# Optimization experiments

Hardware: AMD Instinct MI355X
Metric: run time of the kernel (lower is better)

## Reference

```python
import jax, jax.numpy as jnp
import numpy as np

TOP_K = 2
AUX_COEF = 0.001


def setup_inputs() -> dict:
    key = jax.random.key(0)
    ks = jax.random.split(key, 5)
    B, S, H, I, E = 4, 2048, 1024, 4096, 8
    return {
        "hidden_states": jax.random.normal(ks[0], (B, S, H), dtype=jnp.float32),
        "router_w": jax.random.normal(ks[1], (H, E), dtype=jnp.float32) * 0.02,
        "w_gate": jax.random.normal(ks[2], (E, H, I), dtype=jnp.float32) * 0.02,
        "w_up": jax.random.normal(ks[3], (E, H, I), dtype=jnp.float32) * 0.02,
        "w_down": jax.random.normal(ks[4], (E, I, H), dtype=jnp.float32) * 0.02,
    }


def reference(hidden_states, router_w, w_gate, w_up, w_down):
    B, S, H = hidden_states.shape
    E = router_w.shape[1]
    x = jnp.clip(hidden_states, -10.0, 10.0)          # [B,S,H]
    xf = x.reshape(-1, H)                              # [T,H]
    T = xf.shape[0]

    # --- token-choice router (fp32) ---
    logits = xf.astype(jnp.float32) @ router_w         # [T,E]
    z_loss = jnp.mean(jax.nn.logsumexp(logits, axis=-1) ** 2)
    probs = jax.nn.softmax(logits, axis=-1)            # [T,E]
    top_w, top_i = jax.lax.top_k(probs, TOP_K)         # [T,K]
    top_w = top_w / jnp.sum(top_w, axis=-1, keepdims=True)
    # load-balance loss: aux * E * sum_e f_e * P_e
    assign = jax.nn.one_hot(top_i, E, dtype=jnp.float32).sum(axis=1)  # [T,E]
    frac_tokens = assign.mean(axis=0) / TOP_K
    mean_probs = probs.mean(axis=0)
    lb_loss = AUX_COEF * E * jnp.sum(frac_tokens * mean_probs)

    # --- dense per-expert SwiGLU MLP, then gather selected outputs ---
    expert_outs = []
    for e in range(E):  # small fixed loop over experts
        gate = xf @ w_gate[e]                          # [T,I]
        up = xf @ w_up[e]                              # [T,I]
        expert_outs.append((jax.nn.silu(gate) * up) @ w_down[e])  # [T,H]
    outs = jnp.stack(expert_outs, axis=0)              # [E,T,H]

    gathered = outs[top_i, jnp.arange(T)[:, None], :]  # [T,K,H]
    out = jnp.einsum("tk,tkh->th", top_w.astype(x.dtype), gathered)
    out = jnp.clip(out, -10.0, 10.0).reshape(B, S, H)
    return out, lb_loss, z_loss
```

## Files before the change

### kernel.cpp

```cpp
#include <hip/hip_runtime.h>
#include <stdint.h>

#define TOKENS 8192
#define HDIM 1024
#define IDIM 4096
#define NEXP 8
#define MPAD 17408
#define MTILES 136

typedef float f32x4 __attribute__((ext_vector_type(4)));
typedef __bf16 bf16x8 __attribute__((ext_vector_type(8)));

static __device__ __forceinline__ uint16_t f2bf(float f) {
  uint32_t u = __builtin_bit_cast(uint32_t, f);
  return (uint16_t)((u + 0x7fffu + ((u >> 16) & 1u)) >> 16);
}
static __device__ __forceinline__ uint32_t pack2(float a, float b) {
  return (uint32_t)f2bf(a) | ((uint32_t)f2bf(b) << 16);
}
static __device__ __forceinline__ float bf2f(uint32_t h) {
  return __builtin_bit_cast(float, h << 16);
}
#define SWZ(r) (((r) ^ ((r) >> 3)) & 7u)
static __device__ __forceinline__ void load_lds16(const void* g, void* l) {
  __builtin_amdgcn_global_load_lds(
      (const __attribute__((address_space(1))) uint32_t*)(uintptr_t)g,
      (__attribute__((address_space(3))) uint32_t*)(uintptr_t)l, 16, 0, 0);
}

__global__ __launch_bounds__(256) void router_kernel(
    const float* __restrict__ x, const float* __restrict__ rw,
    uint16_t* __restrict__ xb, float2* __restrict__ topw, int2* __restrict__ tope,
    int* __restrict__ cnt_slots, float* __restrict__ psum_slots, float* __restrict__ zsum_slots) {
  const int tid = threadIdx.x;
  const int lane = tid & 63, wid = tid >> 6;
  const int t = blockIdx.x * 4 + wid;

  const float* xrow = x + (size_t)t * HDIM + lane * 16;
  float xc[16];
#pragma unroll
  for (int i = 0; i < 4; ++i) {
    float4 v = *(const float4*)(xrow + i * 4);
    xc[i * 4 + 0] = fminf(fmaxf(v.x, -10.f), 10.f);
    xc[i * 4 + 1] = fminf(fmaxf(v.y, -10.f), 10.f);
    xc[i * 4 + 2] = fminf(fmaxf(v.z, -10.f), 10.f);
    xc[i * 4 + 3] = fminf(fmaxf(v.w, -10.f), 10.f);
  }
  uint4 o0, o1;
  o0.x = pack2(xc[0], xc[1]);   o0.y = pack2(xc[2], xc[3]);
  o0.z = pack2(xc[4], xc[5]);   o0.w = pack2(xc[6], xc[7]);
  o1.x = pack2(xc[8], xc[9]);   o1.y = pack2(xc[10], xc[11]);
  o1.z = pack2(xc[12], xc[13]); o1.w = pack2(xc[14], xc[15]);
  uint4* dst = (uint4*)(xb + (size_t)t * HDIM + lane * 16);
  dst[0] = o0; dst[1] = o1;

  float acc[8];
#pragma unroll
  for (int e = 0; e < 8; ++e) acc[e] = 0.f;
  const float* rwp = rw + (size_t)(lane * 16) * NEXP;
#pragma unroll
  for (int i = 0; i < 16; ++i) {
    float xi = xc[i];
    float4 a = *(const float4*)(rwp + i * 8);
    float4 b = *(const float4*)(rwp + i * 8 + 4);
    acc[0] += xi * a.x; acc[1] += xi * a.y; acc[2] += xi * a.z; acc[3] += xi * a.w;
    acc[4] += xi * b.x; acc[5] += xi * b.y; acc[6] += xi * b.z; acc[7] += xi * b.w;
  }
#pragma unroll
  for (int s = 1; s < 64; s <<= 1) {
#pragma unroll
    for (int e = 0; e < 8; ++e) acc[e] += __shfl_xor(acc[e], s);
  }

  __shared__ float sp[8]; __shared__ int sc[8]; __shared__ float sz;
  if (tid < 8) { sp[tid] = 0.f; sc[tid] = 0; }
  if (tid == 0) sz = 0.f;
  __syncthreads();

  if (lane == 0) {
    float mx = acc[0];
#pragma unroll
    for (int e = 1; e < 8; ++e) mx = fmaxf(mx, acc[e]);
    float p[8]; float s = 0.f;
#pragma unroll
    for (int e = 0; e < 8; ++e) { p[e] = expf(acc[e] - mx); s += p[e]; }
    float inv = 1.f / s;
#pragma unroll
    for (int e = 0; e < 8; ++e) p[e] *= inv;
    float lse = mx + logf(s);
    int e0 = 0; float b0 = p[0];
#pragma unroll
    for (int e = 1; e < 8; ++e) if (p[e] > b0) { b0 = p[e]; e0 = e; }
    int e1 = (e0 == 0) ? 1 : 0; float b1 = (e0 == 0) ? p[1] : p[0];
#pragma unroll
    for (int e = 0; e < 8; ++e) if (e != e0 && p[e] > b1) { b1 = p[e]; e1 = e; }
    float wn = 1.f / (b0 + b1);
    topw[t] = make_float2(b0 * wn, b1 * wn);
    tope[t] = make_int2(e0, e1);
#pragma unroll
    for (int e = 0; e < 8; ++e) atomicAdd(&sp[e], p[e]);
    atomicAdd(&sc[e0], 1); atomicAdd(&sc[e1], 1);
    atomicAdd(&sz, lse * lse);
  }
  __syncthreads();
  int slot = blockIdx.x & 63;
  if (tid < 8) {
    atomicAdd(&cnt_slots[slot * 8 + tid], sc[tid]);
    atomicAdd(&psum_slots[slot * 8 + tid], sp[tid]);
  }
  if (tid == 0) atomicAdd(&zsum_slots[slot], sz);
}

__global__ void scan_kernel(const int* __restrict__ cnt_slots,
                            const float* __restrict__ psum_slots,
                            const float* __restrict__ zsum_slots,
                            int* __restrict__ seg, int* __restrict__ fill_cnt,
                            float* __restrict__ out_sc) {
  const int tid = threadIdx.x;
  __shared__ int c[8]; __shared__ float ps[8];
  if (tid < 8) {
    int s = 0; float f = 0.f;
    for (int k = 0; k < 64; ++k) { s += cnt_slots[k * 8 + tid]; f += psum_slots[k * 8 + tid]; }
    c[tid] = s; ps[tid] = f; fill_cnt[tid] = 0;
  }
  __syncthreads();
  if (tid == 0) {
    int off = 0;
    for (int e = 0; e < 8; ++e) { seg[e] = off; off += (c[e] + 127) & ~127; }
    seg[8] = off;
    float lb = 0.f;
    for (int e = 0; e < 8; ++e)
      lb += ((float)c[e] / (2.0f * (float)TOKENS)) * (ps[e] / (float)TOKENS);
    lb *= 0.001f * (float)NEXP;
    float z = 0.f;
    for (int k = 0; k < 64; ++k) z += zsum_slots[k];
    out_sc[0] = lb;
    out_sc[1] = z / (float)TOKENS;
  }
}

__global__ __launch_bounds__(256) void fill_kernel(
    const int2* __restrict__ tope, const int* __restrict__ seg,
    int* __restrict__ fill_cnt, int* __restrict__ rowtok) {
  const int t = blockIdx.x * 256 + threadIdx.x;
  const int lane = threadIdx.x & 63;
  const int2 te = tope[t];
#pragma unroll
  for (int k = 0; k < 2; ++k) {
    const int e = k ? te.y : te.x;
    int pos = 0;
    for (int ee = 0; ee < 8; ++ee) {
      unsigned long long mask = __ballot(e == ee);
      if (e == ee) {
        unsigned long long below = mask & ((lane == 0) ? 0ull : (~0ull >> (64 - lane)));
        int nbelow = __popcll(below);
        int leader = __ffsll((unsigned long long)mask) - 1;
        int base = 0;
        if (lane == leader) base = atomicAdd(&fill_cnt[ee], __popcll(mask));
        base = __shfl(base, leader);
        pos = seg[ee] + base + nbelow;
      }
    }
    rowtok[pos] = t * 2 + k;
  }
}

__global__ __launch_bounds__(256) void convert_kernel(
    const float* __restrict__ w_gate, const float* __restrict__ w_up,
    const float* __restrict__ w_down, uint16_t* __restrict__ wgT,
    uint16_t* __restrict__ wuT, uint16_t* __restrict__ wdT) {
  __shared__ uint64_t tt[64][17];
  const int tid = threadIdx.x;
  const int z = blockIdx.y;
  const int bx = blockIdx.x;
  const float* src; uint16_t* dst; int R, C, tr, tc;
  if (z < 16) {
    R = 1024; C = 4096; tr = bx >> 6; tc = bx & 63;
    int e = z & 7;
    src = (z < 8 ? w_gate : w_up) + (size_t)e * 1024 * 4096;
    dst = (z < 8 ? wgT : wuT) + (size_t)e * 1024 * 4096;
  } else {
    R = 4096; C = 1024; tr = bx >> 4; tc = bx & 15;
    int e = z - 16;
    src = w_down + (size_t)e * 4096 * 1024;
    dst = wdT + (size_t)e * 4096 * 1024;
  }
  const int i = tid >> 4, j = tid & 15;
  float4 v0 = *(const float4*)(src + (size_t)(tr * 64 + 4 * i + 0) * C + tc * 64 + 4 * j);
  float4 v1 = *(const float4*)(src + (size_t)(tr * 64 + 4 * i + 1) * C + tc * 64 + 4 * j);
  float4 v2 = *(const float4*)(src + (size_t)(tr * 64 + 4 * i + 2) * C + tc * 64 + 4 * j);
  float4 v3 = *(const float4*)(src + (size_t)(tr * 64 + 4 * i + 3) * C + tc * 64 + 4 * j);
  tt[4 * j + 0][i] = (uint64_t)pack2(v0.x, v1.x) | ((uint64_t)pack2(v2.x, v3.x) << 32);
  tt[4 * j + 1][i] = (uint64_t)pack2(v0.y, v1.y) | ((uint64_t)pack2(v2.y, v3.y) << 32);
  tt[4 * j + 2][i] = (uint64_t)pack2(v0.z, v1.z) | ((uint64_t)pack2(v2.z, v3.z) << 32);
  tt[4 * j + 3][i] = (uint64_t)pack2(v0.w, v1.w) | ((uint64_t)pack2(v2.w, v3.w) << 32);
  __syncthreads();
#pragma unroll
  for (int it = 0; it < 2; ++it) {
    int idx = it * 256 + tid;
    int c = idx >> 3, h = idx & 7;
    uint64_t a = tt[c][2 * h], b = tt[c][2 * h + 1];
    uint4 v;
    v.x = (uint32_t)a; v.y = (uint32_t)(a >> 32);
    v.z = (uint32_t)b; v.w = (uint32_t)(b >> 32);
    *(uint4*)(dst + (size_t)(tc * 64 + c) * R + tr * 64 + h * 8) = v;
  }
}

static __device__ __forceinline__ int xcd_swz(int b, int nwg) {
  int q = nwg >> 3, r = nwg & 7;
  int xcd = b & 7;
  int base = (xcd < r) ? xcd * (q + 1) : r * (q + 1) + (xcd - r) * q;
  return base + (b >> 3);
}

__global__ __launch_bounds__(256, 2) void gemm1_kernel(
    const uint16_t* __restrict__ xb, const uint16_t* __restrict__ wgT,
    const uint16_t* __restrict__ wuT, const int* __restrict__ rowtok,
    const int* __restrict__ seg, uint16_t* __restrict__ hbuf, int mt0) {
  __shared__ __align__(16) char smem[49152];
  const int tid = threadIdx.x;
  const int lane = tid & 63, wid = tid >> 6;
  const int ct = (int)gridDim.y;
  const int b = (int)(blockIdx.y * gridDim.x + blockIdx.x);
  const int wg_lin = xcd_swz(b, 32 * ct);
  const int iblk = wg_lin / ct;
  const int mrel = wg_lin % ct;
  const int mtile = mt0 + mrel;
  const int row0 = mtile * 128;
  if (row0 >= seg[8]) return;
  int e = 0;
  while (row0 >= seg[e + 1]) ++e;
  const uint16_t* wgp = wgT + (size_t)e * HDIM * IDIM;
  const uint16_t* wup = wuT + (size_t)e * HDIM * IDIM;
  const int icol0 = iblk * 128;

  const uint32_t c8 = lane & 7;
  uintptr_t asrc[4], gsrc[4], usrc[4];
#pragma unroll
  for (int j = 0; j < 4; ++j) {
    uint32_t m = (uint32_t)(wid * 32 + j * 8 + (lane >> 3));
    int rt = rowtok[row0 + m];
    int tok = (rt < 0) ? 0 : (rt >> 1);
    uint32_t sw = (c8 ^ SWZ(m)) * 16;
    asrc[j] = (uintptr_t)(xb + (size_t)tok * HDIM) + sw;
    gsrc[j] = (uintptr_t)(wgp + (size_t)(icol0 + m) * HDIM) + sw;
    usrc[j] = (uintptr_t)(wup + (size_t)(icol0 + m) * HDIM) + sw;
  }

  f32x4 accg[4][4] = {}; f32x4 accu[4][4] = {};

  for (int kt = 0; kt < HDIM; kt += 64) {
    __syncthreads();
#pragma unroll
    for (int j = 0; j < 4; ++j) {
      load_lds16((const void*)(asrc[j] + (size_t)kt * 2), smem + wid * 4096 + j * 1024);
      load_lds16((const void*)(gsrc[j] + (size_t)kt * 2), smem + 16384 + wid * 4096 + j * 1024);
      load_lds16((const void*)(usrc[j] + (size_t)kt * 2), smem + 32768 + wid * 4096 + j * 1024);
    }
    __syncthreads();
    const uint32_t g = lane >> 4, l15 = lane & 15;
#pragma unroll
    for (int q = 0; q < 2; ++q) {
      bf16x8 af[4];
#pragma unroll
      for (int mi = 0; mi < 4; ++mi) {
        uint32_t m = (uint32_t)((wid >> 1) * 64 + mi * 16 + l15);
        af[mi] = *(const bf16x8*)(smem + m * 128 + (((uint32_t)(q * 4) + g) ^ SWZ(m)) * 16);
      }
      bf16x8 bg[4], bu[4];
#pragma unroll
      for (int ni = 0; ni < 4; ++ni) {
        uint32_t n = (uint32_t)((wid & 1) * 64 + ni * 16 + l15);
        uint32_t off = n * 128 + (((uint32_t)(q * 4) + g) ^ SWZ(n)) * 16;
        bg[ni] = *(const bf16x8*)(smem + 16384 + off);
        bu[ni] = *(const bf16x8*)(smem + 32768 + off);
      }
#pragma unroll
      for (int mi = 0; mi < 4; ++mi)
#pragma unroll
        for (int ni = 0; ni < 4; ++ni) {
          accg[mi][ni] = __builtin_amdgcn_mfma_f32_16x16x32_bf16(af[mi], bg[ni], accg[mi][ni], 0, 0, 0);
          accu[mi][ni] = __builtin_amdgcn_mfma_f32_16x16x32_bf16(af[mi], bu[ni], accu[mi][ni], 0, 0, 0);
        }
    }
  }
  __syncthreads();
  uint16_t* epi = (uint16_t*)smem;
  const int wr = wid >> 1, wc = wid & 1;
#pragma unroll
  for (int mi = 0; mi < 4; ++mi)
#pragma unroll
    for (int ni = 0; ni < 4; ++ni)
#pragma unroll
      for (int r = 0; r < 4; ++r) {
        float gv = accg[mi][ni][r], uv = accu[mi][ni][r];
        float hv = gv * uv * __frcp_rn(1.0f + __expf(-gv));
        int m = wr * 64 + mi * 16 + (lane >> 4) * 4 + r;
        int n = wc * 64 + ni * 16 + (lane & 15);
        epi[m * 136 + n] = f2bf(hv);
      }
  __syncthreads();
  const int hrow0 = (mtile - mt0) * 128;
  const int m = tid >> 1;
#pragma unroll
  for (int j = 0; j < 8; ++j) {
    int ch = (tid & 1) + j * 2;
    uint4 v = *(const uint4*)(smem + m * 272 + ch * 16);
    *(uint4*)(hbuf + ((size_t)(hrow0 + m)) * IDIM + icol0 + ch * 8) = v;
  }
}

__global__ __launch_bounds__(256, 2) void gemm2_kernel(
    const uint16_t* __restrict__ hbuf, const uint16_t* __restrict__ wdT,
    const int* __restrict__ rowtok, const int* __restrict__ seg,
    uint16_t* __restrict__ pairbuf, int mt0) {
  __shared__ __align__(16) char smem[34816];
  const int tid = threadIdx.x;
  const int lane = tid & 63, wid = tid >> 6;
  const int ct = (int)gridDim.y;
  const int b = (int)(blockIdx.y * gridDim.x + blockIdx.x);
  const int wg_lin = xcd_swz(b, 8 * ct);
  const int nblk = wg_lin / ct;
  const int mrel = wg_lin % ct;
  const int mtile = mt0 + mrel;
  const int row0 = mtile * 128;
  if (row0 >= seg[8]) return;
  int e = 0;
  while (row0 >= seg[e + 1]) ++e;
  const uint16_t* wdp = wdT + (size_t)e * IDIM * HDIM;
  const int ncol0 = nblk * 128;
  const int hrow0 = (mtile - mt0) * 128;

  const uint32_t c8 = lane & 7;
  uintptr_t asrc[4], bsrc[4];
#pragma unroll
  for (int j = 0; j < 4; ++j) {
    uint32_t m = (uint32_t)(wid * 32 + j * 8 + (lane >> 3));
    uint32_t sw = (c8 ^ SWZ(m)) * 16;
    asrc[j] = (uintptr_t)(hbuf + (size_t)(hrow0 + m) * IDIM) + sw;
    bsrc[j] = (uintptr_t)(wdp + (size_t)(ncol0 + m) * IDIM) + sw;
  }

  f32x4 acc[4][4] = {};

  for (int kt = 0; kt < IDIM; kt += 64) {
    __syncthreads();
#pragma unroll
    for (int j = 0; j < 4; ++j) {
      load_lds16((const void*)(asrc[j] + (size_t)kt * 2), smem + wid * 4096 + j * 1024);
      load_lds16((const void*)(bsrc[j] + (size_t)kt * 2), smem + 16384 + wid * 4096 + j * 1024);
    }
    __syncthreads();
    const uint32_t g = lane >> 4, l15 = lane & 15;
#pragma unroll
    for (int q = 0; q < 2; ++q) {
      bf16x8 af[4];
#pragma unroll
      for (int mi = 0; mi < 4; ++mi) {
        uint32_t m = (uint32_t)((wid >> 1) * 64 + mi * 16 + l15);
        af[mi] = *(const bf16x8*)(smem + m * 128 + (((uint32_t)(q * 4) + g) ^ SWZ(m)) * 16);
      }
      bf16x8 bf[4];
#pragma unroll
      for (int ni = 0; ni < 4; ++ni) {
        uint32_t n = (uint32_t)((wid & 1) * 64 + ni * 16 + l15);
        bf[ni] = *(const bf16x8*)(smem + 16384 + n * 128 + (((uint32_t)(q * 4) + g) ^ SWZ(n)) * 16);
      }
#pragma unroll
      for (int mi = 0; mi < 4; ++mi)
#pragma unroll
        for (int ni = 0; ni < 4; ++ni)
          acc[mi][ni] = __builtin_amdgcn_mfma_f32_16x16x32_bf16(af[mi], bf[ni], acc[mi][ni], 0, 0, 0);
    }
  }
  __syncthreads();
  uint16_t* epi = (uint16_t*)smem;
  const int wr = wid >> 1, wc = wid & 1;
#pragma unroll
  for (int mi = 0; mi < 4; ++mi)
#pragma unroll
    for (int ni = 0; ni < 4; ++ni)
#pragma unroll
      for (int r = 0; r < 4; ++r) {
        int m = wr * 64 + mi * 16 + (lane >> 4) * 4 + r;
        int n = wc * 64 + ni * 16 + (lane & 15);
        epi[m * 136 + n] = f2bf(acc[mi][ni][r]);
      }
  __syncthreads();
  const int m = tid >> 1;
  const int rt = rowtok[row0 + m];
  if (rt >= 0) {
#pragma unroll
    for (int j = 0; j < 8; ++j) {
      int ch = (tid & 1) + j * 2;
      uint4 v = *(const uint4*)(smem + m * 272 + ch * 16);
      *(uint4*)(pairbuf + (size_t)rt * HDIM + ncol0 + ch * 8) = v;
    }
  }
}

__global__ __launch_bounds__(256) void combine_kernel(
    const uint16_t* __restrict__ pairbuf, const float2* __restrict__ topw,
    float* __restrict__ out) {
  size_t i = (size_t)blockIdx.x * 256 + threadIdx.x;
  int t = (int)(i >> 7);
  int ch = (int)(i & 127);
  float2 w = topw[t];
  const uint16_t* p0 = pairbuf + (size_t)(t * 2) * HDIM + ch * 8;
  uint4 a = *(const uint4*)p0;
  uint4 b = *(const uint4*)(p0 + HDIM);
  float o[8];
  uint32_t au[4] = {a.x, a.y, a.z, a.w};
  uint32_t bu[4] = {b.x, b.y, b.z, b.w};
#pragma unroll
  for (int j = 0; j < 4; ++j) {
    float v0 = w.x * bf2f(au[j] & 0xffffu) + w.y * bf2f(bu[j] & 0xffffu);
    float v1 = w.x * bf2f(au[j] >> 16) + w.y * bf2f(bu[j] >> 16);
    o[j * 2 + 0] = fminf(fmaxf(v0, -10.f), 10.f);
    o[j * 2 + 1] = fminf(fmaxf(v1, -10.f), 10.f);
  }
  float* op = out + (size_t)t * HDIM + ch * 8;
  float4 w0 = {o[0], o[1], o[2], o[3]};
  float4 w1 = {o[4], o[5], o[6], o[7]};
  *(float4*)op = w0;
  *(float4*)(op + 4) = w1;
}

extern "C" void kernel_launch(void* const* d_in, const int* in_sizes, int n_in,
                              void* d_out, int out_size, void* d_ws, size_t ws_size,
                              hipStream_t stream) {
  (void)in_sizes; (void)n_in; (void)out_size;
  const float* x = (const float*)d_in[0];
  const float* rw = (const float*)d_in[1];
  const float* w_gate = (const float*)d_in[2];
  const float* w_up = (const float*)d_in[3];
  const float* w_down = (const float*)d_in[4];
  float* out = (float*)d_out;

  char* ws = (char*)d_ws;
  size_t off = 0;
  auto alloc = [&](size_t n) { char* p = ws + off; off += (n + 255) & ~(size_t)255; return p; };
  uint16_t* xb = (uint16_t*)alloc((size_t)TOKENS * HDIM * 2);
  float2* topw = (float2*)alloc((size_t)TOKENS * 8);
  int2* tope = (int2*)alloc((size_t)TOKENS * 8);
  int* rowtok = (int*)alloc((size_t)MPAD * 4);
  int* seg = (int*)alloc(16 * 4);
  int* fill_cnt = (int*)alloc(8 * 4);
  int* cnt_slots = (int*)alloc(64 * 8 * 4);
  float* psum_slots = (float*)alloc(64 * 8 * 4);
  float* zsum_slots = (float*)alloc(64 * 4);
  uint16_t* pairbuf = (uint16_t*)alloc((size_t)TOKENS * 2 * HDIM * 2);
  uint16_t* wgT = (uint16_t*)alloc((size_t)NEXP * HDIM * IDIM * 2);
  uint16_t* wuT = (uint16_t*)alloc((size_t)NEXP * HDIM * IDIM * 2);
  uint16_t* wdT = (uint16_t*)alloc((size_t)NEXP * IDIM * HDIM * 2);
  uint16_t* hbuf = (uint16_t*)(ws + off);
  size_t avail = (ws_size > off) ? (ws_size - off) : 0;
  long tiles_fit = (long)(avail / (128ull * IDIM * 2));
  int chunk = (tiles_fit >= MTILES) ? MTILES : (tiles_fit < 1 ? 1 : (int)tiles_fit);

  hipMemsetAsync(cnt_slots, 0, 64 * 8 * 4, stream);
  hipMemsetAsync(psum_slots, 0, 64 * 8 * 4, stream);
  hipMemsetAsync(zsum_slots, 0, 64 * 4, stream);
  hipMemsetAsync(rowtok, 0xFF, (size_t)MPAD * 4, stream);

  convert_kernel<<<dim3(1024, 24), 256, 0, stream>>>(w_gate, w_up, w_down, wgT, wuT, wdT);
  router_kernel<<<TOKENS / 4, 256, 0, stream>>>(x, rw, xb, topw, tope,
                                                cnt_slots, psum_slots, zsum_slots);
  scan_kernel<<<1, 64, 0, stream>>>(cnt_slots, psum_slots, zsum_slots, seg, fill_cnt,
                                    out + (size_t)TOKENS * HDIM);
  fill_kernel<<<TOKENS / 256, 256, 0, stream>>>(tope, seg, fill_cnt, rowtok);

  for (int mt0 = 0; mt0 < MTILES; mt0 += chunk) {
    int ct = (MTILES - mt0 < chunk) ? (MTILES - mt0) : chunk;
    gemm1_kernel<<<dim3(IDIM / 128, ct), 256, 0, stream>>>(xb, wgT, wuT, rowtok, seg, hbuf, mt0);
    gemm2_kernel<<<dim3(HDIM / 128, ct), 256, 0, stream>>>(hbuf, wdT, rowtok, seg, pairbuf, mt0);
  }
  combine_kernel<<<(TOKENS * HDIM / 8) / 256, 256, 0, stream>>>(pairbuf, topw, out);
}
```

Baseline: 740.3 us.

## Double-buffer LDS tiles with async global_load_lds prefetch in both expert GEMMs

Replaces the single-buffered K=64 load/sync/compute loops in the gate-up and down GEMMs with a two-stage ping-pong pipeline over K=32 tiles. The next tile is issued with global_load_lds right after fragments are read, using vmcnt waits and raw barriers, and s_setprio is raised around the MFMA block. The LDS swizzle changes to a 4-chunk pattern to fit the narrower 64-byte rows. The aim is to hide global memory latency behind MFMA work. The cost is more barriers per unit of K and tighter manual scheduling, which must be correct for the buffer-reuse hazards.

```diff
diff --git a/kernel.cpp b/kernel.cpp
--- a/kernel.cpp
+++ b/kernel.cpp
@@ -21,12 +21,19 @@
 static __device__ __forceinline__ float bf2f(uint32_t h) {
   return __builtin_bit_cast(float, h << 16);
 }
-#define SWZ(r) (((r) ^ ((r) >> 3)) & 7u)
+#define SWZ4(r) (((r) >> 1) & 3u)
 static __device__ __forceinline__ void load_lds16(const void* g, void* l) {
   __builtin_amdgcn_global_load_lds(
       (const __attribute__((address_space(1))) uint32_t*)(uintptr_t)g,
       (__attribute__((address_space(3))) uint32_t*)(uintptr_t)l, 16, 0, 0);
 }
+static __device__ __forceinline__ bf16x8 rdfrag(const char* base, uint32_t row, uint32_t g) {
+  return *(const bf16x8*)(base + row * 64 + ((g ^ SWZ4(row)) * 16));
+}
+#define WAITV(n) asm volatile("s_waitcnt vmcnt(" #n ")" ::: "memory")
+#define WAITL0 asm volatile("s_waitcnt lgkmcnt(0)" ::: "memory")
+#define BAR __builtin_amdgcn_s_barrier()
+#define SCHEDB __builtin_amdgcn_sched_barrier(0)
 
 __global__ __launch_bounds__(256) void router_kernel(
     const float* __restrict__ x, const float* __restrict__ rw,
@@ -235,56 +242,78 @@
   const uint16_t* wup = wuT + (size_t)e * HDIM * IDIM;
   const int icol0 = iblk * 128;
 
-  const uint32_t c8 = lane & 7;
-  uintptr_t asrc[4], gsrc[4], usrc[4];
-#pragma unroll
-  for (int j = 0; j < 4; ++j) {
-    uint32_t m = (uint32_t)(wid * 32 + j * 8 + (lane >> 3));
-    int rt = rowtok[row0 + m];
-    int tok = (rt < 0) ? 0 : (rt >> 1);
-    uint32_t sw = (c8 ^ SWZ(m)) * 16;
-    asrc[j] = (uintptr_t)(xb + (size_t)tok * HDIM) + sw;
-    gsrc[j] = (uintptr_t)(wgp + (size_t)(icol0 + m) * HDIM) + sw;
-    usrc[j] = (uintptr_t)(wup + (size_t)(icol0 + m) * HDIM) + sw;
-  }
+  const uint32_t r0 = (uint32_t)(wid * 32 + (lane >> 2));
+  const uint32_t r1 = r0 + 16;
+  const uint32_t cc0 = ((lane & 3u) ^ SWZ4(r0)) * 16;
+  const uint32_t cc1 = ((lane & 3u) ^ SWZ4(r1)) * 16;
+  int rt0 = rowtok[row0 + r0]; int tok0 = (rt0 < 0) ? 0 : (rt0 >> 1);
+  int rt1 = rowtok[row0 + r1]; int tok1 = (rt1 < 0) ? 0 : (rt1 >> 1);
+  const uintptr_t a0 = (uintptr_t)(xb + (size_t)tok0 * HDIM) + cc0;
+  const uintptr_t a1 = (uintptr_t)(xb + (size_t)tok1 * HDIM) + cc1;
+  const uintptr_t g0 = (uintptr_t)(wgp + (size_t)(icol0 + r0) * HDIM) + cc0;
+  const uintptr_t g1 = (uintptr_t)(wgp + (size_t)(icol0 + r1) * HDIM) + cc1;
+  const uintptr_t u0 = (uintptr_t)(wup + (size_t)(icol0 + r0) * HDIM) + cc0;
+  const uintptr_t u1 = (uintptr_t)(wup + (size_t)(icol0 + r1) * HDIM) + cc1;
+  const uint32_t ldsA = (uint32_t)(wid * 2048);
 
   f32x4 accg[4][4] = {}; f32x4 accu[4][4] = {};
 
-  for (int kt = 0; kt < HDIM; kt += 64) {
-    __syncthreads();
-#pragma unroll
-    for (int j = 0; j < 4; ++j) {
-      load_lds16((const void*)(asrc[j] + (size_t)kt * 2), smem + wid * 4096 + j * 1024);
-      load_lds16((const void*)(gsrc[j] + (size_t)kt * 2), smem + 16384 + wid * 4096 + j * 1024);
-      load_lds16((const void*)(usrc[j] + (size_t)kt * 2), smem + 32768 + wid * 4096 + j * 1024);
-    }
-    __syncthreads();
-    const uint32_t g = lane >> 4, l15 = lane & 15;
-#pragma unroll
-    for (int q = 0; q < 2; ++q) {
-      bf16x8 af[4];
-#pragma unroll
-      for (int mi = 0; mi < 4; ++mi) {
-        uint32_t m = (uint32_t)((wid >> 1) * 64 + mi * 16 + l15);
-        af[mi] = *(const bf16x8*)(smem + m * 128 + (((uint32_t)(q * 4) + g) ^ SWZ(m)) * 16);
-      }
-      bf16x8 bg[4], bu[4];
-#pragma unroll
-      for (int ni = 0; ni < 4; ++ni) {
-        uint32_t n = (uint32_t)((wid & 1) * 64 + ni * 16 + l15);
-        uint32_t off = n * 128 + (((uint32_t)(q * 4) + g) ^ SWZ(n)) * 16;
-        bg[ni] = *(const bf16x8*)(smem + 16384 + off);
-        bu[ni] = *(const bf16x8*)(smem + 32768 + off);
-      }
-#pragma unroll
-      for (int mi = 0; mi < 4; ++mi)
-#pragma unroll
-        for (int ni = 0; ni < 4; ++ni) {
-          accg[mi][ni] = __builtin_amdgcn_mfma_f32_16x16x32_bf16(af[mi], bg[ni], accg[mi][ni], 0, 0, 0);
-          accu[mi][ni] = __builtin_amdgcn_mfma_f32_16x16x32_bf16(af[mi], bu[ni], accu[mi][ni], 0, 0, 0);
-        }
-    }
-  }
+#define G1_ISSUE(t, buf)                                                        \
+  {                                                                             \
+    char* B_ = smem + (buf) * 24576;                                            \
+    size_t o_ = (size_t)(t) * 64;                                               \
+    load_lds16((const void*)(a0 + o_), B_ + ldsA);                              \
+    load_lds16((const void*)(a1 + o_), B_ + ldsA + 1024);                       \
+    load_lds16((const void*)(g0 + o_), B_ + 8192 + ldsA);                       \
+    load_lds16((const void*)(g1 + o_), B_ + 8192 + ldsA + 1024);                \
+    load_lds16((const void*)(u0 + o_), B_ + 16384 + ldsA);                      \
+    load_lds16((const void*)(u1 + o_), B_ + 16384 + ldsA + 1024);               \
+  }
+
+  const uint32_t g = lane >> 4, l15 = lane & 15;
+  const uint32_t mrow = (uint32_t)((wid >> 1) * 64) + l15;
+  const uint32_t nrow = (uint32_t)((wid & 1) * 64) + l15;
+
+#define G1_PHASE(buf)                                                           \
+  {                                                                             \
+    const char* B_ = smem + (buf) * 24576;                                      \
+    bf16x8 af[4], bg[4], bu[4];                                                 \
+    _Pragma("unroll") for (int mi = 0; mi < 4; ++mi)                            \
+        af[mi] = rdfrag(B_, mrow + mi * 16, g);                                 \
+    _Pragma("unroll") for (int ni = 0; ni < 4; ++ni) {                          \
+      bg[ni] = rdfrag(B_ + 8192, nrow + ni * 16, g);                            \
+      bu[ni] = rdfrag(B_ + 16384, nrow + ni * 16, g);                           \
+    }                                                                           \
+    WAITL0; SCHEDB;                                                             \
+    BAR; SCHEDB;                                                                \
+    ISSUE_NEXT;                                                                 \
+    SCHEDB;                                                                     \
+    __builtin_amdgcn_s_setprio(1);                                              \
+    _Pragma("unroll") for (int mi = 0; mi < 4; ++mi)                            \
+        _Pragma("unroll") for (int ni = 0; ni < 4; ++ni) {                      \
+      accg[mi][ni] = __builtin_amdgcn_mfma_f32_16x16x32_bf16(af[mi], bg[ni], accg[mi][ni], 0, 0, 0); \
+      accu[mi][ni] = __builtin_amdgcn_mfma_f32_16x16x32_bf16(af[mi], bu[ni], accu[mi][ni], 0, 0, 0); \
+    }                                                                           \
+    __builtin_amdgcn_s_setprio(0);                                              \
+  }
+
+  const int NT = HDIM / 32;
+  WAITV(0);
+  G1_ISSUE(0, 0);
+  G1_ISSUE(1, 1);
+  for (int t = 0; t < NT - 1; ++t) {
+    WAITV(6); BAR; SCHEDB;
+#define ISSUE_NEXT if (t + 2 < NT) G1_ISSUE(t + 2, t & 1)
+    G1_PHASE(t & 1);
+#undef ISSUE_NEXT
+  }
+  {
+    WAITV(0); BAR; SCHEDB;
+#define ISSUE_NEXT
+    G1_PHASE((NT - 1) & 1);
+#undef ISSUE_NEXT
+  }
+
   __syncthreads();
   uint16_t* epi = (uint16_t*)smem;
   const int wr = wid >> 1, wc = wid & 1;
@@ -332,48 +361,68 @@
   const int ncol0 = nblk * 128;
   const int hrow0 = (mtile - mt0) * 128;
 
-  const uint32_t c8 = lane & 7;
-  uintptr_t asrc[4], bsrc[4];
-#pragma unroll
-  for (int j = 0; j < 4; ++j) {
-    uint32_t m = (uint32_t)(wid * 32 + j * 8 + (lane >> 3));
-    uint32_t sw = (c8 ^ SWZ(m)) * 16;
-    asrc[j] = (uintptr_t)(hbuf + (size_t)(hrow0 + m) * IDIM) + sw;
-    bsrc[j] = (uintptr_t)(wdp + (size_t)(ncol0 + m) * IDIM) + sw;
-  }
+  const uint32_t r0 = (uint32_t)(wid * 32 + (lane >> 2));
+  const uint32_t r1 = r0 + 16;
+  const uint32_t cc0 = ((lane & 3u) ^ SWZ4(r0)) * 16;
+  const uint32_t cc1 = ((lane & 3u) ^ SWZ4(r1)) * 16;
+  const uintptr_t a0 = (uintptr_t)(hbuf + (size_t)(hrow0 + r0) * IDIM) + cc0;
+  const uintptr_t a1 = (uintptr_t)(hbuf + (size_t)(hrow0 + r1) * IDIM) + cc1;
+  const uintptr_t b0 = (uintptr_t)(wdp + (size_t)(ncol0 + r0) * IDIM) + cc0;
+  const uintptr_t b1 = (uintptr_t)(wdp + (size_t)(ncol0 + r1) * IDIM) + cc1;
+  const uint32_t ldsA = (uint32_t)(wid * 2048);
 
   f32x4 acc[4][4] = {};
 
-  for (int kt = 0; kt < IDIM; kt += 64) {
-    __syncthreads();
-#pragma unroll
-    for (int j = 0; j < 4; ++j) {
-      load_lds16((const void*)(asrc[j] + (size_t)kt * 2), smem + wid * 4096 + j * 1024);
-      load_lds16((const void*)(bsrc[j] + (size_t)kt * 2), smem + 16384 + wid * 4096 + j * 1024);
-    }
-    __syncthreads();
-    const uint32_t g = lane >> 4, l15 = lane & 15;
-#pragma unroll
-    for (int q = 0; q < 2; ++q) {
-      bf16x8 af[4];
-#pragma unroll
-      for (int mi = 0; mi < 4; ++mi) {
-        uint32_t m = (uint32_t)((wid >> 1) * 64 + mi * 16 + l15);
-        af[mi] = *(const bf16x8*)(smem + m * 128 + (((uint32_t)(q * 4) + g) ^ SWZ(m)) * 16);
-      }
-      bf16x8 bf[4];
-#pragma unroll
-      for (int ni = 0; ni < 4; ++ni) {
-        uint32_t n = (uint32_t)((wid & 1) * 64 + ni * 16 + l15);
-        bf[ni] = *(const bf16x8*)(smem + 16384 + n * 128 + (((uint32_t)(q * 4) + g) ^ SWZ(n)) * 16);
-      }
-#pragma unroll
-      for (int mi = 0; mi < 4; ++mi)
-#pragma unroll
-        for (int ni = 0; ni < 4; ++ni)
-          acc[mi][ni] = __builtin_amdgcn_mfma_f32_16x16x32_bf16(af[mi], bf[ni], acc[mi][ni], 0, 0, 0);
-    }
-  }
+#define G2_ISSUE(t, buf)                                                        \
+  {                                                                             \
+    char* B_ = smem + (buf) * 16384;                                            \
+    size_t o_ = (size_t)(t) * 64;                                               \
+    load_lds16((const void*)(a0 + o_), B_ + ldsA);                              \
+    load_lds16((const void*)(a1 + o_), B_ + ldsA + 1024);                       \
+    load_lds16((const void*)(b0 + o_), B_ + 8192 + ldsA);                       \
+    load_lds16((const void*)(b1 + o_), B_ + 8192 + ldsA + 1024);                \
+  }
+
+  const uint32_t g = lane >> 4, l15 = lane & 15;
+  const uint32_t mrow = (uint32_t)((wid >> 1) * 64) + l15;
+  const uint32_t nrow = (uint32_t)((wid & 1) * 64) + l15;
+
+#define G2_PHASE(buf)                                                           \
+  {                                                                             \
+    const char* B_ = smem + (buf) * 16384;                                      \
+    bf16x8 af[4], bf[4];                                                        \
+    _Pragma("unroll") for (int mi = 0; mi < 4; ++mi)                            \
+        af[mi] = rdfrag(B_, mrow + mi * 16, g);                                 \
+    _Pragma("unroll") for (int ni = 0; ni < 4; ++ni)                            \
+        bf[ni] = rdfrag(B_ + 8192, nrow + ni * 16, g);                          \
+    WAITL0; SCHEDB;                                                             \
+    BAR; SCHEDB;                                                                \
+    ISSUE_NEXT;                                                                 \
+    SCHEDB;                                                                     \
+    __builtin_amdgcn_s_setprio(1);                                              \
+    _Pragma("unroll") for (int mi = 0; mi < 4; ++mi)                            \
+        _Pragma("unroll") for (int ni = 0; ni < 4; ++ni)                        \
+            acc[mi][ni] = __builtin_amdgcn_mfma_f32_16x16x32_bf16(af[mi], bf[ni], acc[mi][ni], 0, 0, 0); \
+    __builtin_amdgcn_s_setprio(0);                                              \
+  }
+
+  const int NT = IDIM / 32;
+  WAITV(0);
+  G2_ISSUE(0, 0);
+  G2_ISSUE(1, 1);
+  for (int t = 0; t < NT - 1; ++t) {
+    WAITV(4); BAR; SCHEDB;
+#define ISSUE_NEXT if (t + 2 < NT) G2_ISSUE(t + 2, t & 1)
+    G2_PHASE(t & 1);
+#undef ISSUE_NEXT
+  }
+  {
+    WAITV(0); BAR; SCHEDB;
+#define ISSUE_NEXT
+    G2_PHASE((NT - 1) & 1);
+#undef ISSUE_NEXT
+  }
+
   __syncthreads();
   uint16_t* epi = (uint16_t*)smem;
   const int wr = wid >> 1, wc = wid & 1;
```

Measured after the change: 717.6 us. 3.1% less time.
